# Kernel optimization log

Measured on AMD Instinct MI355X. Metric: run time of the kernel, lower is better.

Reference implementation:

```python
import jax, jax.numpy as jnp
import numpy as np

B, N, C, H = 2, 2048, 256, 8
HD = C // H
EPS = 1e-5


def _cdist(a, b):
    # a: (B,N,D), b: (B,M,D) -> (B,N,M) euclidean distance (torch.cdist p=2)
    d2 = (jnp.sum(a * a, -1)[:, :, None] + jnp.sum(b * b, -1)[:, None, :]
          - 2.0 * jnp.einsum('bnd,bmd->bnm', a, b))
    return jnp.sqrt(jnp.maximum(d2, 0.0))


def _ln(x, g, b):
    # LayerNorm over last axis
    m = jnp.mean(x, -1, keepdims=True)
    v = jnp.var(x, -1, keepdims=True)
    return (x - m) / jnp.sqrt(v + EPS) * g + b


def _conv1d(x, w, b=None):
    # 1x1 Conv1d: x (B,Cin,N), w (Cout,Cin)
    y = jnp.einsum('oc,bcn->bon', w, x)
    return y if b is None else y + b[:, None]


def setup_inputs() -> dict:
    key = jax.random.key(0)
    ks = jax.random.split(key, 32)
    s = 0.05
    inp = {
        'xyz_A': jax.random.normal(ks[0], (B, N, 3), jnp.float32),
        'featA': jax.random.normal(ks[1], (B, C, N), jnp.float32),
        'xyz_B': jax.random.normal(ks[2], (B, N, 3), jnp.float32),
        'featB': jax.random.normal(ks[3], (B, C, N), jnp.float32),
        # q/k/v projections (Conv1d 1x1)
        'qw': jax.random.normal(ks[4], (C, C), jnp.float32) * s,
        'qb': jnp.zeros((C,), jnp.float32),
        'kw': jax.random.normal(ks[5], (C, C), jnp.float32) * s,
        'kb': jnp.zeros((C,), jnp.float32),
        'vw': jax.random.normal(ks[6], (C, C), jnp.float32) * s,
        'vb': jnp.zeros((C,), jnp.float32),
        # spatial_bias_mlp: Conv2d(1,H/2,1,bias=False) -> BN2d(eval) -> ReLU -> Conv2d(H/2,H,1)
        'sbw1': jax.random.normal(ks[7], (H // 2,), jnp.float32) * s,
        'sbg': jnp.ones((H // 2,), jnp.float32),
        'sbb': jnp.zeros((H // 2,), jnp.float32),
        'sbm': jax.random.normal(ks[8], (H // 2,), jnp.float32) * 0.1,
        'sbv': jax.random.uniform(ks[9], (H // 2,), jnp.float32, 0.5, 1.5),
        'sbw2': jax.random.normal(ks[10], (H, H // 2), jnp.float32) * s,
        'sbb2': jnp.zeros((H,), jnp.float32),
        # dissimilarity projections
        'qdw': jax.random.normal(ks[11], (C, C), jnp.float32) * s,
        'qdb': jnp.zeros((C,), jnp.float32),
        'kdw': jax.random.normal(ks[12], (C, C), jnp.float32) * s,
        'kdb': jnp.zeros((C,), jnp.float32),
        # LayerNorms
        'lin_g': jnp.ones((C,), jnp.float32), 'lin_b': jnp.zeros((C,), jnp.float32),
        'lsim_g': jnp.ones((C,), jnp.float32), 'lsim_b': jnp.zeros((C,), jnp.float32),
        'ldis_g': jnp.ones((C,), jnp.float32), 'ldis_b': jnp.zeros((C,), jnp.float32),
        # fusion MLP: Conv1d(3C,2C,bias=False) -> BN1d(eval) -> ReLU -> Dropout(eval) -> Conv1d(2C,C)
        'fw1': jax.random.normal(ks[13], (2 * C, 3 * C), jnp.float32) * s,
        'fbg': jnp.ones((2 * C,), jnp.float32),
        'fbb': jnp.zeros((2 * C,), jnp.float32),
        'fbm': jax.random.normal(ks[14], (2 * C,), jnp.float32) * 0.1,
        'fbv': jax.random.uniform(ks[15], (2 * C,), jnp.float32, 0.5, 1.5),
        'fw2': jax.random.normal(ks[16], (C, 2 * C), jnp.float32) * s,
        'fb2': jnp.zeros((C,), jnp.float32),
    }
    return inp


def _forward(xyz_A, featA, xyz_B, featB, qw, qb, kw, kb, vw, vb,
             sbw1, sbg, sbb, sbm, sbv, sbw2, sbb2,
             qdw, qdb, kdw, kdb,
             lin_g, lin_b, lsim_g, lsim_b, ldis_g, ldis_b,
             fw1, fbg, fbb, fbm, fbv, fw2, fb2):
    # Pre-norm of featA over channels
    featA_norm = _ln(featA.transpose(0, 2, 1), lin_g, lin_b).transpose(0, 2, 1)  # (B,C,N)

    # Spatial bias: -cdist -> 1x1 conv (in_ch=1) -> BN(eval) -> ReLU -> 1x1 conv
    dist = _cdist(xyz_A, xyz_B)                                # (B,N,N)
    t = jnp.einsum('o,bnm->bonm', sbw1, -dist)                 # (B,H/2,N,N)
    t = (t - sbm[:, None, None]) / jnp.sqrt(sbv + EPS)[:, None, None]
    t = t * sbg[:, None, None] + sbb[:, None, None]
    t = jax.nn.relu(t)
    spatial_bias = jnp.einsum('oh,bhnm->bonm', sbw2, t) + sbb2[:, None, None]  # (B,H,N,N)

    # Similarity path
    q = _conv1d(featA_norm, qw, qb).reshape(B, H, HD, N).transpose(0, 1, 3, 2)  # (B,H,N,hd)
    k = _conv1d(featB, kw, kb).reshape(B, H, HD, N).transpose(0, 1, 3, 2)
    sim_scores = jnp.einsum('bhnd,bhmd->bhnm', q, k) / (HD ** 0.5) + spatial_bias

    # Dissimilarity path: feature cdist + spatial bias
    qd = _conv1d(featA_norm, qdw, qdb).transpose(0, 2, 1)      # (B,N,C)
    kd = _conv1d(featB, kdw, kdb).transpose(0, 2, 1)
    dissim_scores = _cdist(qd, kd)[:, None] + spatial_bias     # (B,H,N,N)

    sim_w = jax.nn.softmax(sim_scores, -1)
    dis_w = jax.nn.softmax(dissim_scores, -1)

    v = _conv1d(featB, vw, vb).reshape(B, H, HD, N).transpose(0, 1, 3, 2)       # (B,H,N,hd)
    ctx_sim = jnp.einsum('bhnm,bhmd->bhnd', sim_w, v).transpose(0, 1, 3, 2).reshape(B, C, N)
    ctx_sim = _ln(ctx_sim.transpose(0, 2, 1), lsim_g, lsim_b).transpose(0, 2, 1)
    ctx_dis = jnp.einsum('bhnm,bhmd->bhnd', dis_w, v).transpose(0, 1, 3, 2).reshape(B, C, N)
    ctx_dis = _ln(ctx_dis.transpose(0, 2, 1), ldis_g, ldis_b).transpose(0, 2, 1)

    fused = jnp.concatenate([featA_norm, ctx_sim, ctx_dis], axis=1)            # (B,3C,N)
    x = jnp.einsum('oc,bcn->bon', fw1, fused)
    x = (x - fbm[:, None]) / jnp.sqrt(fbv + EPS)[:, None] * fbg[:, None] + fbb[:, None]
    x = jax.nn.relu(x)  # Dropout is identity in eval mode
    out = _conv1d(x, fw2, fb2) + featA  # residual_proj is Identity (in==out)
    return out


def reference(xyz_A, featA, xyz_B, featB, qw, qb, kw, kb, vw, vb,
              sbw1, sbg, sbb, sbm, sbv, sbw2, sbb2,
              qdw, qdb, kdw, kdb,
              lin_g, lin_b, lsim_g, lsim_b, ldis_g, ldis_b,
              fw1, fbg, fbb, fbm, fbv, fw2, fb2):
    return _forward(xyz_A, featA, xyz_B, featB, qw, qb, kw, kb, vw, vb,
                    sbw1, sbg, sbb, sbm, sbv, sbw2, sbb2,
                    qdw, qdb, kdw, kdb,
                    lin_g, lin_b, lsim_g, lsim_b, ldis_g, ldis_b,
                    fw1, fbg, fbb, fbm, fbv, fw2, fb2)
```

## Files before the change

kernel.cpp:

```cpp
#include <hip/hip_runtime.h>

#define B_ 2
#define N_ 2048
#define C_ 256
#define H_ 8
#define HD_ 32
#define EPSf 1e-5f

typedef __bf16   bf16x8 __attribute__((ext_vector_type(8)));
typedef float    f32x4  __attribute__((ext_vector_type(4)));
typedef _Float16 f16x8  __attribute__((ext_vector_type(8)));
typedef _Float16 f16x4  __attribute__((ext_vector_type(4)));
typedef _Float16 f16x2  __attribute__((ext_vector_type(2)));

static constexpr size_t MB_ = 1024 * 1024;
static constexpr size_t OFF_FANT = 0;
static constexpr size_t OFF_FBT  = 2 * MB_;
static constexpr size_t OFF_QPK  = 4 * MB_;
static constexpr size_t OFF_KPK  = 6 * MB_;
static constexpr size_t OFF_VPK  = 8 * MB_;
static constexpr size_t OFF_QDT  = 10 * MB_;
static constexpr size_t OFF_KDT  = 12 * MB_;
static constexpr size_t OFF_QQ   = 14 * MB_;
static constexpr size_t OFF_KK   = 14 * MB_ + 16 * 1024;
static constexpr size_t OFF_FDH  = 14 * MB_ + 64 * 1024;
static constexpr size_t OFF_FSD  = 14 * MB_ + 64 * 1024;
static constexpr size_t OFF_CTXS = 31 * MB_;
static constexpr size_t OFF_CTXD = 35 * MB_;
static constexpr size_t OFF_CSLN = 39 * MB_;
static constexpr size_t OFF_CDLN = 41 * MB_;
static constexpr size_t OFF_X1T  = 43 * MB_;
static constexpr size_t WS_NEED  = 47 * MB_;
static constexpr size_t OFF2_CTXS = 47 * MB_;
static constexpr size_t OFF2_CTXD = 51 * MB_;
static constexpr size_t OFF2_CSLN = 55 * MB_;
static constexpr size_t OFF2_CDLN = 57 * MB_;
static constexpr size_t OFF2_X1T  = 59 * MB_;
static constexpr size_t WS_NEED2  = 63 * MB_;

__device__ __forceinline__ float rfl(float x){
  return __uint_as_float(__builtin_amdgcn_readfirstlane(__float_as_uint(x)));
}
__device__ __forceinline__ bf16x8 cvt8(const float* p){
  float4 a = *reinterpret_cast<const float4*>(p);
  float4 c = *reinterpret_cast<const float4*>(p + 4);
  bf16x8 r;
  r[0]=(__bf16)a.x; r[1]=(__bf16)a.y; r[2]=(__bf16)a.z; r[3]=(__bf16)a.w;
  r[4]=(__bf16)c.x; r[5]=(__bf16)c.y; r[6]=(__bf16)c.z; r[7]=(__bf16)c.w;
  return r;
}
__device__ __forceinline__ unsigned int packh2(float lo, float hi){
  f16x2 h; h[0] = (_Float16)lo; h[1] = (_Float16)hi;
  return __builtin_bit_cast(unsigned int, h);
}
__device__ __forceinline__ void unpackh2(unsigned int u, float& lo, float& hi){
  f16x2 h = __builtin_bit_cast(f16x2, u);
  lo = (float)h[0]; hi = (float)h[1];
}

__global__ __launch_bounds__(256) void lnA_pack(const float* __restrict__ featA,
    __bf16* __restrict__ fanT, const float* __restrict__ gam, const float* __restrict__ bet){
  int b = blockIdx.y, n0 = blockIdx.x * 32;
  int t = threadIdx.x, nl = t & 31, cg = t >> 5;
  __shared__ float tile[256][33];
  __shared__ float red1[8][32], red2[8][32], mus[32], rss[32];
  __shared__ float gsh[256], bsh[256];
  gsh[t] = gam[t]; bsh[t] = bet[t];
  #pragma unroll
  for (int i = 0; i < 32; i++){
    int c = cg * 32 + i;
    tile[c][nl] = featA[((size_t)(b * C_ + c)) * N_ + n0 + nl];
  }
  __syncthreads();
  float s1 = 0.f, s2 = 0.f;
  #pragma unroll
  for (int i = 0; i < 32; i++){
    float v = tile[cg * 32 + i][nl];
    s1 += v; s2 += v * v;
  }
  red1[cg][nl] = s1; red2[cg][nl] = s2;
  __syncthreads();
  if (t < 32){
    float a = 0.f, q = 0.f;
    #pragma unroll
    for (int i = 0; i < 8; i++){ a += red1[i][t]; q += red2[i][t]; }
    float m = a / (float)C_;
    mus[t] = m; rss[t] = rsqrtf(q / (float)C_ - m * m + EPSf);
  }
  __syncthreads();
  float mu = mus[nl], rs = rss[nl];
  size_t obase = ((size_t)(b * N_ + n0 + nl)) * C_;
  #pragma unroll
  for (int i = 0; i < 32; i++){
    int c = cg * 32 + i;
    fanT[obase + c] = (__bf16)((tile[c][nl] - mu) * rs * gsh[c] + bsh[c]);
  }
}

__global__ __launch_bounds__(256) void packT_kernel(const float* __restrict__ featB,
    __bf16* __restrict__ fbT){
  int b = blockIdx.z, c0 = blockIdx.y * 64, n0 = blockIdx.x * 64;
  int t = threadIdx.x;
  __shared__ float tile[64][65];
  int cl = t >> 6, nl = t & 63;
  #pragma unroll
  for (int i = 0; i < 16; i++)
    tile[i * 4 + cl][nl] = featB[((size_t)(b * C_ + c0 + i * 4 + cl)) * N_ + n0 + nl];
  __syncthreads();
  int nr = t >> 2, cc = (t & 3) * 16;
  alignas(16) __bf16 tmp[16];
  #pragma unroll
  for (int j = 0; j < 16; j++) tmp[j] = (__bf16)tile[cc + j][nr];
  size_t d = ((size_t)(b * N_ + n0 + nr)) * C_ + c0 + cc;
  *reinterpret_cast<uint4*>(&fbT[d])     = *reinterpret_cast<uint4*>(&tmp[0]);
  *reinterpret_cast<uint4*>(&fbT[d + 8]) = *reinterpret_cast<uint4*>(&tmp[8]);
}

__global__ __launch_bounds__(256) void proj_mfma(const __bf16* __restrict__ fanT,
    const __bf16* __restrict__ fbT, __bf16* __restrict__ wsh, int vfp16,
    const float* __restrict__ qw, const float* __restrict__ qb,
    const float* __restrict__ kw, const float* __restrict__ kb,
    const float* __restrict__ vw, const float* __restrict__ vb,
    const float* __restrict__ qdw, const float* __restrict__ qdb,
    const float* __restrict__ kdw, const float* __restrict__ kdb){
  const int p = blockIdx.z % 5, b = blockIdx.z / 5;
  const int t = threadIdx.x, w = t >> 6, lane = t & 63, ln = lane & 15, g = lane >> 4;
  const float *W, *bias;
  const __bf16* X;
  __bf16* Y;
  if (p == 0)      { W = qw;  bias = qb;  X = fanT; Y = wsh + (OFF_QPK - OFF_FANT) / 2; }
  else if (p == 1) { W = kw;  bias = kb;  X = fbT;  Y = wsh + (OFF_KPK - OFF_FANT) / 2; }
  else if (p == 2) { W = vw;  bias = vb;  X = fbT;  Y = wsh + (OFF_VPK - OFF_FANT) / 2; }
  else if (p == 3) { W = qdw; bias = qdb; X = fanT; Y = wsh + (OFF_QDT - OFF_FANT) / 2; }
  else             { W = kdw; bias = kdb; X = fbT;  Y = wsh + (OFF_KDT - OFF_FANT) / 2; }

  f32x4 acc[4];
  #pragma unroll
  for (int i = 0; i < 4; i++) acc[i] = (f32x4){0.f, 0.f, 0.f, 0.f};

  if (p != 2){
    const int n0w = blockIdx.x * 64 + w * 16, o0 = blockIdx.y * 64;
    #pragma unroll
    for (int ks = 0; ks < 8; ks++){
      bf16x8 af = *reinterpret_cast<const bf16x8*>(
          &X[((size_t)(b * N_ + n0w + ln)) * C_ + ks * 32 + g * 8]);
      #pragma unroll
      for (int ot = 0; ot < 4; ot++){
        bf16x8 bf = cvt8(&W[(size_t)(o0 + ot * 16 + ln) * C_ + ks * 32 + g * 8]);
        acc[ot] = __builtin_amdgcn_mfma_f32_16x16x32_bf16(af, bf, acc[ot], 0, 0, 0);
      }
    }
    const float inv = 0.17677669529663687f;
    #pragma unroll
    for (int ot = 0; ot < 4; ot++){
      int o = o0 + ot * 16 + ln;
      float bz = bias[o];
      #pragma unroll
      for (int r = 0; r < 4; r++){
        int n = n0w + g * 4 + r;
        float val = acc[ot][r] + bz;
        if (p == 0){
          val *= inv;
          Y[(((size_t)(b * H_ + (o >> 5))) * N_ + n) * HD_ + (o & 31)] = (__bf16)val;
        } else if (p == 1){
          Y[(((size_t)(b * H_ + (o >> 5))) * N_ + n) * HD_ + (o & 31)] = (__bf16)val;
        } else {
          Y[((size_t)(b * N_ + n)) * C_ + o] = (__bf16)val;
        }
      }
    }
  } else {
    const int o0w = blockIdx.y * 64 + w * 16, n0 = blockIdx.x * 64;
    #pragma unroll
    for (int ks = 0; ks < 8; ks++){
      bf16x8 af = cvt8(&W[(size_t)(o0w + ln) * C_ + ks * 32 + g * 8]);
      #pragma unroll
      for (int nt = 0; nt < 4; nt++){
        bf16x8 bf = *reinterpret_cast<const bf16x8*>(
            &X[((size_t)(b * N_ + n0 + nt * 16 + ln)) * C_ + ks * 32 + g * 8]);
        acc[nt] = __builtin_amdgcn_mfma_f32_16x16x32_bf16(af, bf, acc[nt], 0, 0, 0);
      }
    }
    float bz[4];
    #pragma unroll
    for (int r = 0; r < 4; r++) bz[r] = vb[o0w + g * 4 + r];
    #pragma unroll
    for (int nt = 0; nt < 4; nt++)
      #pragma unroll
      for (int r = 0; r < 4; r++){
        int o = o0w + g * 4 + r, n = n0 + nt * 16 + ln;
        size_t idx = ((size_t)(b * C_ + o)) * N_ + n;
        float val = acc[nt][r] + bz[r];
        if (vfp16) ((_Float16*)Y)[idx] = (_Float16)val;
        else       Y[idx] = (__bf16)val;
      }
  }
}

__global__ __launch_bounds__(256) void norms_b(const __bf16* __restrict__ qdT,
    const __bf16* __restrict__ kdT, float* __restrict__ qq, float* __restrict__ kk){
  int b = blockIdx.y, n = blockIdx.x * 64 + (threadIdx.x >> 2), part = threadIdx.x & 3;
  size_t base = ((size_t)(b * N_ + n)) * C_ + part * 64;
  float s1 = 0.f, s2 = 0.f;
  #pragma unroll
  for (int i = 0; i < 8; i++){
    bf16x8 a = *reinterpret_cast<const bf16x8*>(&qdT[base + i * 8]);
    bf16x8 d = *reinterpret_cast<const bf16x8*>(&kdT[base + i * 8]);
    #pragma unroll
    for (int j = 0; j < 8; j++){
      float fa = (float)a[j]; s1 += fa * fa;
      float fd = (float)d[j]; s2 += fd * fd;
    }
  }
  s1 += __shfl_xor(s1, 1); s1 += __shfl_xor(s1, 2);
  s2 += __shfl_xor(s2, 1); s2 += __shfl_xor(s2, 2);
  if (part == 0){ qq[b * N_ + n] = s1; kk[b * N_ + n] = s2; }
}

__global__ __launch_bounds__(256) void pairdist_mfma(const __bf16* __restrict__ qdT,
    const __bf16* __restrict__ kdT, const float* __restrict__ qq,
    const float* __restrict__ kk, const float* __restrict__ xyzA,
    const float* __restrict__ xyzB, unsigned int* __restrict__ fsd){
  const int t = threadIdx.x, w = t >> 6, lane = t & 63, ln = lane & 15, g = lane >> 4;
  const int b = blockIdx.z, n0 = blockIdx.y * 64, n0w = n0 + w * 16, m0 = blockIdx.x * 64;
  __shared__ float4 xa[64], xb[64];
  __shared__ unsigned int sbl[4][16][68];

  if (t < 64){
    const float* p = &xyzA[((size_t)(b * N_ + n0 + t)) * 3];
    xa[t] = make_float4(p[0], p[1], p[2], 0.f);
  } else if (t < 128){
    const float* p = &xyzB[((size_t)(b * N_ + m0 + t - 64)) * 3];
    xb[t - 64] = make_float4(p[0], p[1], p[2], 0.f);
  }
  bf16x8 qfr[8];
  #pragma unroll
  for (int ks = 0; ks < 8; ks++)
    qfr[ks] = *reinterpret_cast<const bf16x8*>(
        &qdT[((size_t)(b * N_ + n0w + ln)) * C_ + ks * 32 + g * 8]);
  float qqv[4];
  #pragma unroll
  for (int r = 0; r < 4; r++) qqv[r] = qq[b * N_ + n0w + g * 4 + r];
  __syncthreads();
  float4 xav[4];
  #pragma unroll
  for (int r = 0; r < 4; r++) xav[r] = xa[w * 16 + g * 4 + r];

  #pragma unroll
  for (int mt = 0; mt < 4; mt++){
    f32x4 a = (f32x4){0.f, 0.f, 0.f, 0.f};
    #pragma unroll
    for (int ks = 0; ks < 8; ks++){
      bf16x8 kfr = *reinterpret_cast<const bf16x8*>(
          &kdT[((size_t)(b * N_ + m0 + mt * 16 + ln)) * C_ + ks * 32 + g * 8]);
      a = __builtin_amdgcn_mfma_f32_16x16x32_bf16(qfr[ks], kfr, a, 0, 0, 0);
    }
    float kkv = kk[b * N_ + m0 + mt * 16 + ln];
    float4 xbv = xb[mt * 16 + ln];
    #pragma unroll
    for (int r = 0; r < 4; r++){
      float d2 = qqv[r] + kkv - 2.f * a[r];
      float fd = sqrtf(fmaxf(d2, 0.f));
      float dx = xav[r].x - xbv.x, dy = xav[r].y - xbv.y, dz = xav[r].z - xbv.z;
      float sd = sqrtf(dx * dx + dy * dy + dz * dz);
      sbl[w][g * 4 + r][mt * 16 + ln] = packh2(fd, sd);
    }
  }
  #pragma unroll
  for (int it = 0; it < 4; it++){
    int row = it * 4 + (lane >> 4), cq = lane & 15;
    uint4 v = *reinterpret_cast<const uint4*>(&sbl[w][row][cq * 4]);
    *reinterpret_cast<uint4*>(&fsd[((size_t)(b * N_ + n0w + row)) * N_ + m0 + cq * 4]) = v;
  }
}

__global__ __launch_bounds__(256) void dual_attn2(
    const __bf16* __restrict__ qpk, const __bf16* __restrict__ kpk,
    const _Float16* __restrict__ vph, const unsigned int* __restrict__ fsd,
    const float* __restrict__ sbw1, const float* __restrict__ sbg, const float* __restrict__ sbb,
    const float* __restrict__ sbm, const float* __restrict__ sbv,
    const float* __restrict__ sbw2, const float* __restrict__ sbb2,
    float* __restrict__ ctxsT, float* __restrict__ ctxdT){
  const int t = threadIdx.x, w = t >> 6, lane = t & 63, ln = lane & 15, g = lane >> 4;
  const int h = blockIdx.y, b = blockIdx.z;
  const int nbase = blockIdx.x * 64 + w * 16;
  const int n = nbase + ln;

  float Ac[4], Bc[4], W2h[4];
  #pragma unroll
  for (int j = 0; j < 4; j++){
    float rs = rsqrtf(sbv[j] + EPSf);
    Ac[j]  = rfl(-sbw1[j] * rs * sbg[j]);
    Bc[j]  = rfl(-sbm[j] * rs * sbg[j] + sbb[j]);
    W2h[j] = rfl(sbw2[h * 4 + j]);
  }
  float C0 = rfl(sbb2[h]);

  bf16x8 qf = *reinterpret_cast<const bf16x8*>(
      &qpk[(((size_t)(b * H_ + h)) * N_ + n) * HD_ + g * 8]);
  const unsigned int* fsdrow = &fsd[((size_t)(b * N_ + n)) * N_];
  const _Float16* vbase = &vph[((size_t)(b * C_ + h * HD_)) * N_];

  f32x4 os[2], od[2];
  #pragma unroll
  for (int i = 0; i < 2; i++){ os[i] = (f32x4){0.f,0.f,0.f,0.f}; od[i] = (f32x4){0.f,0.f,0.f,0.f}; }
  float ms = -3e38f, ls = 0.f, md = -3e38f, ld = 0.f;

  for (int m0 = 0; m0 < N_; m0 += 64){
    f32x4 sa[4];
    #pragma unroll
    for (int mt = 0; mt < 4; mt++){
      bf16x8 kf = *reinterpret_cast<const bf16x8*>(
          &kpk[(((size_t)(b * H_ + h)) * N_ + m0 + mt * 16 + ln) * HD_ + g * 8]);
      f32x4 z = (f32x4){0.f, 0.f, 0.f, 0.f};
      sa[mt] = __builtin_amdgcn_mfma_f32_16x16x32_bf16(kf, qf, z, 0, 0, 0);
    }
    float sv[16], dv[16];
    float mxs = -3e38f, mxd = -3e38f;
    #pragma unroll
    for (int mt = 0; mt < 4; mt++){
      uint4 fu = *reinterpret_cast<const uint4*>(&fsdrow[m0 + mt * 16 + g * 4]);
      #pragma unroll
      for (int r = 0; r < 4; r++){
        unsigned int uu = (r == 0) ? fu.x : (r == 1) ? fu.y : (r == 2) ? fu.z : fu.w;
        float fd, sd;
        unpackh2(uu, fd, sd);
        float u0 = fmaxf(fmaf(Ac[0], sd, Bc[0]), 0.f);
        float u1 = fmaxf(fmaf(Ac[1], sd, Bc[1]), 0.f);
        float u2 = fmaxf(fmaf(Ac[2], sd, Bc[2]), 0.f);
        float u3 = fmaxf(fmaf(Ac[3], sd, Bc[3]), 0.f);
        float bias = C0 + W2h[0] * u0 + W2h[1] * u1 + W2h[2] * u2 + W2h[3] * u3;
        float s = sa[mt][r] + bias;
        float d = fd + bias;
        sv[mt * 4 + r] = s; dv[mt * 4 + r] = d;
        mxs = fmaxf(mxs, s); mxd = fmaxf(mxd, d);
      }
    }
    mxs = fmaxf(mxs, __shfl_xor(mxs, 16)); mxs = fmaxf(mxs, __shfl_xor(mxs, 32));
    mxd = fmaxf(mxd, __shfl_xor(mxd, 16)); mxd = fmaxf(mxd, __shfl_xor(mxd, 32));
    float nms = fmaxf(ms, mxs), als = __expf(ms - nms);
    float nmd = fmaxf(md, mxd), ald = __expf(md - nmd);
    f16x4 pAs[4], pAd[4];
    float pss = 0.f, psd = 0.f;
    #pragma unroll
    for (int mt = 0; mt < 4; mt++)
      #pragma unroll
      for (int r = 0; r < 4; r++){
        float pv = __expf(sv[mt * 4 + r] - nms); pss += pv; pAs[mt][r] = (_Float16)pv;
        float qv = __expf(dv[mt * 4 + r] - nmd); psd += qv; pAd[mt][r] = (_Float16)qv;
      }
    pss += __shfl_xor(pss, 16); pss += __shfl_xor(pss, 32);
    psd += __shfl_xor(psd, 16); psd += __shfl_xor(psd, 32);
    ls = ls * als + pss; ms = nms;
    ld = ld * ald + psd; md = nmd;
    float alsr[4], aldr[4];
    #pragma unroll
    for (int r = 0; r < 4; r++){
      alsr[r] = __shfl(als, g * 4 + r);
      aldr[r] = __shfl(ald, g * 4 + r);
    }
    #pragma unroll
    for (int dt = 0; dt < 2; dt++)
      #pragma unroll
      for (int r = 0; r < 4; r++){ os[dt][r] *= alsr[r]; od[dt][r] *= aldr[r]; }
    #pragma unroll
    for (int mt = 0; mt < 4; mt++){
      #pragma unroll
      for (int dt = 0; dt < 2; dt++){
        f16x4 vf = *reinterpret_cast<const f16x4*>(
            &vbase[(size_t)(dt * 16 + ln) * N_ + m0 + mt * 16 + g * 4]);
        os[dt] = __builtin_amdgcn_mfma_f32_16x16x16f16(pAs[mt], vf, os[dt], 0, 0, 0);
        od[dt] = __builtin_amdgcn_mfma_f32_16x16x16f16(pAd[mt], vf, od[dt], 0, 0, 0);
      }
    }
  }
  float is = 1.f / ls, idd = 1.f / ld;
  float isr[4], idr[4];
  #pragma unroll
  for (int r = 0; r < 4; r++){
    isr[r] = __shfl(is, g * 4 + r);
    idr[r] = __shfl(idd, g * 4 + r);
  }
  #pragma unroll
  for (int dt = 0; dt < 2; dt++)
    #pragma unroll
    for (int r = 0; r < 4; r++){
      int nn = nbase + g * 4 + r;
      int ch = h * HD_ + dt * 16 + ln;
      size_t base = ((size_t)(b * N_ + nn)) * C_ + ch;
      ctxsT[base] = os[dt][r] * isr[r];
      ctxdT[base] = od[dt][r] * idr[r];
    }
}

__global__ __launch_bounds__(256) void fdist_mfma(const __bf16* __restrict__ qdT,
    const __bf16* __restrict__ kdT, const float* __restrict__ qq,
    const float* __restrict__ kk, _Float16* __restrict__ fdh){
  const int t = threadIdx.x, w = t >> 6, lane = t & 63, ln = lane & 15, g = lane >> 4;
  const int b = blockIdx.z, n0 = blockIdx.y * 64 + w * 16, m0 = blockIdx.x * 64;
  __shared__ _Float16 sbl[4][16][68];

  bf16x8 qfr[8];
  #pragma unroll
  for (int ks = 0; ks < 8; ks++)
    qfr[ks] = *reinterpret_cast<const bf16x8*>(
        &qdT[((size_t)(b * N_ + n0 + ln)) * C_ + ks * 32 + g * 8]);
  float qqv[4];
  #pragma unroll
  for (int r = 0; r < 4; r++) qqv[r] = qq[b * N_ + n0 + g * 4 + r];

  #pragma unroll
  for (int mt = 0; mt < 4; mt++){
    f32x4 a = (f32x4){0.f, 0.f, 0.f, 0.f};
    #pragma unroll
    for (int ks = 0; ks < 8; ks++){
      bf16x8 kfr = *reinterpret_cast<const bf16x8*>(
          &kdT[((size_t)(b * N_ + m0 + mt * 16 + ln)) * C_ + ks * 32 + g * 8]);
      a = __builtin_amdgcn_mfma_f32_16x16x32_bf16(qfr[ks], kfr, a, 0, 0, 0);
    }
    float kkv = kk[b * N_ + m0 + mt * 16 + ln];
    #pragma unroll
    for (int r = 0; r < 4; r++){
      float d2 = qqv[r] + kkv - 2.f * a[r];
      sbl[w][g * 4 + r][mt * 16 + ln] = (_Float16)sqrtf(fmaxf(d2, 0.f));
    }
  }
  __syncthreads();
  #pragma unroll
  for (int it = 0; it < 8; it++){
    int row = (lane >> 5) + it * 2, colu = lane & 31;
    unsigned int u = *reinterpret_cast<const unsigned int*>(&sbl[w][row][colu * 2]);
    *reinterpret_cast<unsigned int*>(&fdh[((size_t)(b * N_ + n0 + row)) * N_ + m0 + colu * 2]) = u;
  }
}

__global__ __launch_bounds__(256) void dual_attn(
    const __bf16* __restrict__ qpk, const __bf16* __restrict__ kpk, const __bf16* __restrict__ vpk,
    const _Float16* __restrict__ fdh,
    const float* __restrict__ xyzA, const float* __restrict__ xyzB,
    const float* __restrict__ sbw1, const float* __restrict__ sbg, const float* __restrict__ sbb,
    const float* __restrict__ sbm, const float* __restrict__ sbv,
    const float* __restrict__ sbw2, const float* __restrict__ sbb2,
    float* __restrict__ ctxsT, float* __restrict__ ctxdT){
  const int t = threadIdx.x, w = t >> 6, lane = t & 63, ln = lane & 15, g = lane >> 4;
  const int h = blockIdx.y, b = blockIdx.z;
  const int nbase = blockIdx.x * 64 + w * 16;
  const int n = nbase + ln;

  float Ac[4], Bc[4], W2h[4];
  #pragma unroll
  for (int j = 0; j < 4; j++){
    float rs = rsqrtf(sbv[j] + EPSf);
    Ac[j]  = rfl(-sbw1[j] * rs * sbg[j]);
    Bc[j]  = rfl(-sbm[j] * rs * sbg[j] + sbb[j]);
    W2h[j] = rfl(sbw2[h * 4 + j]);
  }
  float C0 = rfl(sbb2[h]);

  bf16x8 qf = *reinterpret_cast<const bf16x8*>(
      &qpk[(((size_t)(b * H_ + h)) * N_ + n) * HD_ + g * 8]);
  float ax = xyzA[((size_t)(b * N_ + n)) * 3 + 0];
  float ay = xyzA[((size_t)(b * N_ + n)) * 3 + 1];
  float az = xyzA[((size_t)(b * N_ + n)) * 3 + 2];
  const _Float16* fdrow = &fdh[((size_t)(b * N_ + n)) * N_];

  f32x4 os[2], od[2];
  #pragma unroll
  for (int i = 0; i < 2; i++){ os[i] = (f32x4){0.f,0.f,0.f,0.f}; od[i] = (f32x4){0.f,0.f,0.f,0.f}; }
  float ms = -3e38f, ls = 0.f, md = -3e38f, ld = 0.f;

  __shared__ __align__(16) float ss[4][16][68];
  __shared__ float4 xbb[4][64];

  for (int m0 = 0; m0 < N_; m0 += 64){
    __syncthreads();
    {
      const float* xp = &xyzB[((size_t)(b * N_ + m0 + lane)) * 3];
      xbb[w][lane] = make_float4(xp[0], xp[1], xp[2], 0.f);
    }
    f32x4 sa[4];
    #pragma unroll
    for (int i = 0; i < 4; i++) sa[i] = (f32x4){0.f, 0.f, 0.f, 0.f};
    #pragma unroll
    for (int mt = 0; mt < 4; mt++){
      bf16x8 kf = *reinterpret_cast<const bf16x8*>(
          &kpk[(((size_t)(b * H_ + h)) * N_ + m0 + mt * 16 + ln) * HD_ + g * 8]);
      sa[mt] = __builtin_amdgcn_mfma_f32_16x16x32_bf16(qf, kf, sa[mt], 0, 0, 0);
    }
    #pragma unroll
    for (int mt = 0; mt < 4; mt++)
      #pragma unroll
      for (int r = 0; r < 4; r++)
        ss[w][g * 4 + r][mt * 16 + ln] = sa[mt][r];
    __syncthreads();

    #pragma unroll
    for (int kh = 0; kh < 2; kh++){
      float s8[8], d8[8];
      {
        float4 A4 = *reinterpret_cast<const float4*>(&ss[w][ln][kh * 32 + g * 8]);
        float4 B4 = *reinterpret_cast<const float4*>(&ss[w][ln][kh * 32 + g * 8 + 4]);
        s8[0]=A4.x; s8[1]=A4.y; s8[2]=A4.z; s8[3]=A4.w;
        s8[4]=B4.x; s8[5]=B4.y; s8[6]=B4.z; s8[7]=B4.w;
      }
      f16x8 fv = *reinterpret_cast<const f16x8*>(&fdrow[m0 + kh * 32 + g * 8]);
      float mxs = -3e38f, mxd = -3e38f;
      #pragma unroll
      for (int j = 0; j < 8; j++){
        float4 xk = xbb[w][kh * 32 + g * 8 + j];
        float dx = ax - xk.x, dy = ay - xk.y, dz = az - xk.z;
        float sd = sqrtf(dx * dx + dy * dy + dz * dz);
        float bias = C0;
        #pragma unroll
        for (int u = 0; u < 4; u++)
          bias += W2h[u] * fmaxf(fmaf(Ac[u], sd, Bc[u]), 0.f);
        s8[j] += bias;
        d8[j] = (float)fv[j] + bias;
        mxs = fmaxf(mxs, s8[j]);
        mxd = fmaxf(mxd, d8[j]);
      }
      mxs = fmaxf(mxs, __shfl_xor(mxs, 16)); mxs = fmaxf(mxs, __shfl_xor(mxs, 32));
      mxd = fmaxf(mxd, __shfl_xor(mxd, 16)); mxd = fmaxf(mxd, __shfl_xor(mxd, 32));
      float nms = fmaxf(ms, mxs), als = __expf(ms - nms);
      float nmd = fmaxf(md, mxd), ald = __expf(md - nmd);
      float pss = 0.f, psd = 0.f;
      bf16x8 pfs, pfd;
      #pragma unroll
      for (int j = 0; j < 8; j++){
        float pv = __expf(s8[j] - nms); pss += pv; pfs[j] = (__bf16)pv;
        float qv = __expf(d8[j] - nmd); psd += qv; pfd[j] = (__bf16)qv;
      }
      pss += __shfl_xor(pss, 16); pss += __shfl_xor(pss, 32);
      psd += __shfl_xor(psd, 16); psd += __shfl_xor(psd, 32);
      ls = ls * als + pss; ms = nms;
      ld = ld * ald + psd; md = nmd;
      os[0] *= als; os[1] *= als; od[0] *= ald; od[1] *= ald;
      #pragma unroll
      for (int dt = 0; dt < 2; dt++){
        bf16x8 vf = *reinterpret_cast<const bf16x8*>(
            &vpk[((size_t)(b * C_ + h * HD_ + dt * 16 + ln)) * N_ + m0 + kh * 32 + g * 8]);
        os[dt] = __builtin_amdgcn_mfma_f32_16x16x32_bf16(vf, pfs, os[dt], 0, 0, 0);
        od[dt] = __builtin_amdgcn_mfma_f32_16x16x32_bf16(vf, pfd, od[dt], 0, 0, 0);
      }
    }
  }
  float is = 1.f / ls, idv = 1.f / ld;
  #pragma unroll
  for (int dt = 0; dt < 2; dt++)
    #pragma unroll
    for (int r = 0; r < 4; r++){
      int ch = h * HD_ + dt * 16 + g * 4 + r;
      size_t base = ((size_t)(b * N_ + n)) * C_ + ch;
      ctxsT[base] = os[dt][r] * is;
      ctxdT[base] = od[dt][r] * idv;
    }
}

__global__ __launch_bounds__(256) void ln_ctx(const float* __restrict__ ctxsT,
    const float* __restrict__ ctxdT, __bf16* __restrict__ csLN, __bf16* __restrict__ cdLN,
    const float* __restrict__ lsg, const float* __restrict__ lsb,
    const float* __restrict__ ldg, const float* __restrict__ ldb){
  const float* src = blockIdx.y ? ctxdT : ctxsT;
  __bf16* dst = blockIdx.y ? cdLN : csLN;
  const float* gg = blockIdx.y ? ldg : lsg;
  const float* bb = blockIdx.y ? ldb : lsb;
  int w = threadIdx.x >> 6, lane = threadIdx.x & 63;
  size_t row = (size_t)blockIdx.x * 4 + w;
  float4 v = *reinterpret_cast<const float4*>(&src[row * C_ + lane * 4]);
  float s1 = v.x + v.y + v.z + v.w;
  float s2 = v.x * v.x + v.y * v.y + v.z * v.z + v.w * v.w;
  #pragma unroll
  for (int off = 1; off < 64; off <<= 1){
    s1 += __shfl_xor(s1, off);
    s2 += __shfl_xor(s2, off);
  }
  float m = s1 / (float)C_;
  float rs = rsqrtf(s2 / (float)C_ - m * m + EPSf);
  float4 g4 = *reinterpret_cast<const float4*>(&gg[lane * 4]);
  float4 b4 = *reinterpret_cast<const float4*>(&bb[lane * 4]);
  alignas(8) __bf16 o4[4];
  o4[0] = (__bf16)((v.x - m) * rs * g4.x + b4.x);
  o4[1] = (__bf16)((v.y - m) * rs * g4.y + b4.y);
  o4[2] = (__bf16)((v.z - m) * rs * g4.z + b4.z);
  o4[3] = (__bf16)((v.w - m) * rs * g4.w + b4.w);
  *reinterpret_cast<uint2*>(&dst[row * C_ + lane * 4]) = *reinterpret_cast<uint2*>(o4);
}

__global__ __launch_bounds__(256) void fusion1_mfma(const __bf16* __restrict__ fanT,
    const __bf16* __restrict__ csLN, const __bf16* __restrict__ cdLN,
    __bf16* __restrict__ X1T, const float* __restrict__ fw1,
    const float* __restrict__ fbg, const float* __restrict__ fbb,
    const float* __restrict__ fbm, const float* __restrict__ fbv){
  const int t = threadIdx.x, w = t >> 6, lane = t & 63, ln = lane & 15, g = lane >> 4;
  const int b = blockIdx.z, o0 = blockIdx.y * 64, n0w = blockIdx.x * 64 + w * 16;
  f32x4 acc[4];
  #pragma unroll
  for (int i = 0; i < 4; i++) acc[i] = (f32x4){0.f, 0.f, 0.f, 0.f};
  const __bf16* segs[3] = {fanT, csLN, cdLN};
  #pragma unroll
  for (int ks = 0; ks < 24; ks++){
    const __bf16* base = segs[ks >> 3];
    int coff = (ks & 7) * 32 + g * 8;
    bf16x8 af = *reinterpret_cast<const bf16x8*>(
        &base[((size_t)(b * N_ + n0w + ln)) * C_ + coff]);
    #pragma unroll
    for (int ot = 0; ot < 4; ot++){
      bf16x8 bf = cvt8(&fw1[(size_t)(o0 + ot * 16 + ln) * (3 * C_) + ks * 32 + g * 8]);
      acc[ot] = __builtin_amdgcn_mfma_f32_16x16x32_bf16(af, bf, acc[ot], 0, 0, 0);
    }
  }
  #pragma unroll
  for (int ot = 0; ot < 4; ot++){
    int o = o0 + ot * 16 + ln;
    float mn = fbm[o], rs = rsqrtf(fbv[o] + EPSf), gg = fbg[o], be = fbb[o];
    #pragma unroll
    for (int r = 0; r < 4; r++){
      int n = n0w + g * 4 + r;
      float x = (acc[ot][r] - mn) * rs * gg + be;
      X1T[((size_t)(b * N_ + n)) * (2 * C_) + o] = (__bf16)fmaxf(x, 0.f);
    }
  }
}

__global__ __launch_bounds__(256) void fusion2_mfma(const __bf16* __restrict__ X1T,
    const float* __restrict__ fw2, const float* __restrict__ fb2,
    const float* __restrict__ featA, float* __restrict__ out){
  const int t = threadIdx.x, w = t >> 6, lane = t & 63, ln = lane & 15, g = lane >> 4;
  const int b = blockIdx.z, o0w = blockIdx.y * 64 + w * 16, n0 = blockIdx.x * 64;
  f32x4 acc[4];
  #pragma unroll
  for (int i = 0; i < 4; i++) acc[i] = (f32x4){0.f, 0.f, 0.f, 0.f};
  #pragma unroll
  for (int ks = 0; ks < 16; ks++){
    bf16x8 af = cvt8(&fw2[(size_t)(o0w + ln) * (2 * C_) + ks * 32 + g * 8]);
    #pragma unroll
    for (int nt = 0; nt < 4; nt++){
      bf16x8 bf = *reinterpret_cast<const bf16x8*>(
          &X1T[((size_t)(b * N_ + n0 + nt * 16 + ln)) * (2 * C_) + ks * 32 + g * 8]);
      acc[nt] = __builtin_amdgcn_mfma_f32_16x16x32_bf16(af, bf, acc[nt], 0, 0, 0);
    }
  }
  float bz[4];
  #pragma unroll
  for (int r = 0; r < 4; r++) bz[r] = fb2[o0w + g * 4 + r];
  #pragma unroll
  for (int nt = 0; nt < 4; nt++)
    #pragma unroll
    for (int r = 0; r < 4; r++){
      int o = o0w + g * 4 + r, n = n0 + nt * 16 + ln;
      size_t oi = ((size_t)(b * C_ + o)) * N_ + n;
      out[oi] = acc[nt][r] + bz[r] + featA[oi];
    }
}

extern "C" void kernel_launch(void* const* d_in, const int* in_sizes, int n_in,
                              void* d_out, int out_size, void* d_ws, size_t ws_size,
                              hipStream_t stream){
  (void)in_sizes; (void)n_in; (void)out_size;
  if (ws_size < WS_NEED) return;

  const float* xyzA  = (const float*)d_in[0];
  const float* featA = (const float*)d_in[1];
  const float* xyzB  = (const float*)d_in[2];
  const float* featB = (const float*)d_in[3];
  const float* qw  = (const float*)d_in[4];   const float* qb  = (const float*)d_in[5];
  const float* kw  = (const float*)d_in[6];   const float* kb  = (const float*)d_in[7];
  const float* vw  = (const float*)d_in[8];   const float* vb  = (const float*)d_in[9];
  const float* sbw1= (const float*)d_in[10];  const float* sbg = (const float*)d_in[11];
  const float* sbb = (const float*)d_in[12];  const float* sbm = (const float*)d_in[13];
  const float* sbv = (const float*)d_in[14];  const float* sbw2= (const float*)d_in[15];
  const float* sbb2= (const float*)d_in[16];
  const float* qdw = (const float*)d_in[17];  const float* qdb = (const float*)d_in[18];
  const float* kdw = (const float*)d_in[19];  const float* kdb = (const float*)d_in[20];
  const float* ling= (const float*)d_in[21];  const float* linb= (const float*)d_in[22];
  const float* lsg = (const float*)d_in[23];  const float* lsb = (const float*)d_in[24];
  const float* ldg = (const float*)d_in[25];  const float* ldb = (const float*)d_in[26];
  const float* fw1 = (const float*)d_in[27];  const float* fbg = (const float*)d_in[28];
  const float* fbb = (const float*)d_in[29];  const float* fbm = (const float*)d_in[30];
  const float* fbv = (const float*)d_in[31];  const float* fw2 = (const float*)d_in[32];
  const float* fb2 = (const float*)d_in[33];

  char* ws = (char*)d_ws;
  __bf16*   fanT = (__bf16*)(ws + OFF_FANT);
  __bf16*   fbT  = (__bf16*)(ws + OFF_FBT);
  __bf16*   qpk  = (__bf16*)(ws + OFF_QPK);
  __bf16*   kpk  = (__bf16*)(ws + OFF_KPK);
  __bf16*   qdT  = (__bf16*)(ws + OFF_QDT);
  __bf16*   kdT  = (__bf16*)(ws + OFF_KDT);
  float*    qq   = (float*)(ws + OFF_QQ);
  float*    kk   = (float*)(ws + OFF_KK);
  float*    out  = (float*)d_out;

  bool big = (ws_size >= WS_NEED2);

  lnA_pack<<<dim3(N_ / 32, B_), 256, 0, stream>>>(featA, fanT, ling, linb);
  packT_kernel<<<dim3(N_ / 64, C_ / 64, B_), 256, 0, stream>>>(featB, fbT);
  proj_mfma<<<dim3(N_ / 64, C_ / 64, 5 * B_), 256, 0, stream>>>(
      fanT, fbT, fanT, big ? 1 : 0, qw, qb, kw, kb, vw, vb, qdw, qdb, kdw, kdb);
  norms_b<<<dim3(N_ / 64, B_), 256, 0, stream>>>(qdT, kdT, qq, kk);

  if (big){
    _Float16*     vph  = (_Float16*)(ws + OFF_VPK);
    unsigned int* fsd  = (unsigned int*)(ws + OFF_FSD);
    float*  ctxsT = (float*)(ws + OFF2_CTXS);
    float*  ctxdT = (float*)(ws + OFF2_CTXD);
    __bf16* csLN  = (__bf16*)(ws + OFF2_CSLN);
    __bf16* cdLN  = (__bf16*)(ws + OFF2_CDLN);
    __bf16* X1T   = (__bf16*)(ws + OFF2_X1T);
    pairdist_mfma<<<dim3(N_ / 64, N_ / 64, B_), 256, 0, stream>>>(
        qdT, kdT, qq, kk, xyzA, xyzB, fsd);
    dual_attn2<<<dim3(N_ / 64, H_, B_), 256, 0, stream>>>(
        qpk, kpk, vph, fsd, sbw1, sbg, sbb, sbm, sbv, sbw2, sbb2, ctxsT, ctxdT);
    ln_ctx<<<dim3(B_ * N_ / 4, 2), 256, 0, stream>>>(
        ctxsT, ctxdT, csLN, cdLN, lsg, lsb, ldg, ldb);
    fusion1_mfma<<<dim3(N_ / 64, (2 * C_) / 64, B_), 256, 0, stream>>>(
        fanT, csLN, cdLN, X1T, fw1, fbg, fbb, fbm, fbv);
    fusion2_mfma<<<dim3(N_ / 64, C_ / 64, B_), 256, 0, stream>>>(
        X1T, fw2, fb2, featA, out);
  } else {
    __bf16*   vpk  = (__bf16*)(ws + OFF_VPK);
    _Float16* fdh  = (_Float16*)(ws + OFF_FDH);
    float*  ctxsT = (float*)(ws + OFF_CTXS);
    float*  ctxdT = (float*)(ws + OFF_CTXD);
    __bf16* csLN  = (__bf16*)(ws + OFF_CSLN);
    __bf16* cdLN  = (__bf16*)(ws + OFF_CDLN);
    __bf16* X1T   = (__bf16*)(ws + OFF_X1T);
    fdist_mfma<<<dim3(N_ / 64, N_ / 64, B_), 256, 0, stream>>>(qdT, kdT, qq, kk, fdh);
    dual_attn<<<dim3(N_ / 64, H_, B_), 256, 0, stream>>>(
        qpk, kpk, vpk, fdh, xyzA, xyzB,
        sbw1, sbg, sbb, sbm, sbv, sbw2, sbb2, ctxsT, ctxdT);
    ln_ctx<<<dim3(B_ * N_ / 4, 2), 256, 0, stream>>>(
        ctxsT, ctxdT, csLN, cdLN, lsg, lsb, ldg, ldb);
    fusion1_mfma<<<dim3(N_ / 64, (2 * C_) / 64, B_), 256, 0, stream>>>(
        fanT, csLN, cdLN, X1T, fw1, fbg, fbb, fbm, fbv);
    fusion2_mfma<<<dim3(N_ / 64, C_ / 64, B_), 256, 0, stream>>>(
        X1T, fw2, fb2, featA, out);
  }
}
```

Measured before the change: 291.1 us.

## Split attention key range in two with register double-buffering and merged combine+LayerNorm

```diff
diff --git a/kernel.cpp b/kernel.cpp
--- a/kernel.cpp
+++ b/kernel.cpp
@@ -31,12 +31,13 @@
 static constexpr size_t OFF_CDLN = 41 * MB_;
 static constexpr size_t OFF_X1T  = 43 * MB_;
 static constexpr size_t WS_NEED  = 47 * MB_;
-static constexpr size_t OFF2_CTXS = 47 * MB_;
-static constexpr size_t OFF2_CTXD = 51 * MB_;
-static constexpr size_t OFF2_CSLN = 55 * MB_;
-static constexpr size_t OFF2_CDLN = 57 * MB_;
-static constexpr size_t OFF2_X1T  = 59 * MB_;
-static constexpr size_t WS_NEED2  = 63 * MB_;
+static constexpr size_t OFF2_PART  = 47 * MB_;
+static constexpr size_t OFF2_STATM = 55 * MB_;
+static constexpr size_t OFF2_STATL = 56 * MB_;
+static constexpr size_t OFF2_CSLN  = 15 * MB_;
+static constexpr size_t OFF2_CDLN  = 17 * MB_;
+static constexpr size_t OFF2_X1T   = 19 * MB_;
+static constexpr size_t WS_NEED2   = 63 * MB_;
 
 __device__ __forceinline__ float rfl(float x){
   return __uint_as_float(__builtin_amdgcn_readfirstlane(__float_as_uint(x)));
@@ -274,17 +275,104 @@
   }
 }
 
-__global__ __launch_bounds__(256) void dual_attn2(
+struct TileRegs { uint4 fu[4]; bf16x8 kf[4]; };
+
+__device__ __forceinline__ void load_tile(TileRegs& T, const __bf16* kbase,
+    const unsigned int* fsdrow, int m0, int ln, int g){
+  #pragma unroll
+  for (int mt = 0; mt < 4; mt++){
+    T.fu[mt] = *reinterpret_cast<const uint4*>(&fsdrow[m0 + mt * 16 + g * 4]);
+    T.kf[mt] = *reinterpret_cast<const bf16x8*>(&kbase[(size_t)(m0 + mt * 16 + ln) * HD_ + g * 8]);
+  }
+}
+
+__device__ __forceinline__ void compute_tile(const TileRegs& T,
+    const _Float16* vbase, int m0, int ln, int g, bf16x8 qf,
+    const float* Ac, const float* Bc, const float* W2h, float C0,
+    f32x4* os, f32x4* od, float& ms, float& ls, float& md, float& ld){
+  f32x4 sa[4];
+  #pragma unroll
+  for (int mt = 0; mt < 4; mt++){
+    f32x4 z = (f32x4){0.f, 0.f, 0.f, 0.f};
+    sa[mt] = __builtin_amdgcn_mfma_f32_16x16x32_bf16(T.kf[mt], qf, z, 0, 0, 0);
+  }
+  f16x4 vf[2][4];
+  #pragma unroll
+  for (int mt = 0; mt < 4; mt++)
+    #pragma unroll
+    for (int dt = 0; dt < 2; dt++)
+      vf[dt][mt] = *reinterpret_cast<const f16x4*>(
+          &vbase[(size_t)(dt * 16 + ln) * N_ + m0 + mt * 16 + g * 4]);
+  f32x4 dvv[4];
+  float mxs = -3e38f, mxd = -3e38f;
+  #pragma unroll
+  for (int mt = 0; mt < 4; mt++){
+    #pragma unroll
+    for (int r = 0; r < 4; r++){
+      unsigned int uu = (r == 0) ? T.fu[mt].x : (r == 1) ? T.fu[mt].y
+                      : (r == 2) ? T.fu[mt].z : T.fu[mt].w;
+      float fd, sd;
+      unpackh2(uu, fd, sd);
+      float u0 = fmaxf(fmaf(Ac[0], sd, Bc[0]), 0.f);
+      float u1 = fmaxf(fmaf(Ac[1], sd, Bc[1]), 0.f);
+      float u2 = fmaxf(fmaf(Ac[2], sd, Bc[2]), 0.f);
+      float u3 = fmaxf(fmaf(Ac[3], sd, Bc[3]), 0.f);
+      float bias = C0 + W2h[0] * u0 + W2h[1] * u1 + W2h[2] * u2 + W2h[3] * u3;
+      float s = sa[mt][r] + bias;
+      float d = fd + bias;
+      sa[mt][r] = s; dvv[mt][r] = d;
+      mxs = fmaxf(mxs, s); mxd = fmaxf(mxd, d);
+    }
+  }
+  mxs = fmaxf(mxs, __shfl_xor(mxs, 16)); mxs = fmaxf(mxs, __shfl_xor(mxs, 32));
+  mxd = fmaxf(mxd, __shfl_xor(mxd, 16)); mxd = fmaxf(mxd, __shfl_xor(mxd, 32));
+  float nms = fmaxf(ms, mxs), als = __expf(ms - nms);
+  float nmd = fmaxf(md, mxd), ald = __expf(md - nmd);
+  f16x4 pAs[4], pAd[4];
+  float pss = 0.f, psd = 0.f;
+  #pragma unroll
+  for (int mt = 0; mt < 4; mt++)
+    #pragma unroll
+    for (int r = 0; r < 4; r++){
+      float pv = __expf(sa[mt][r] - nms); pss += pv; pAs[mt][r] = (_Float16)pv;
+      float qv = __expf(dvv[mt][r] - nmd); psd += qv; pAd[mt][r] = (_Float16)qv;
+    }
+  pss += __shfl_xor(pss, 16); pss += __shfl_xor(pss, 32);
+  psd += __shfl_xor(psd, 16); psd += __shfl_xor(psd, 32);
+  ls = ls * als + pss; ms = nms;
+  ld = ld * ald + psd; md = nmd;
+  float alsr[4], aldr[4];
+  #pragma unroll
+  for (int r = 0; r < 4; r++){
+    alsr[r] = __shfl(als, g * 4 + r);
+    aldr[r] = __shfl(ald, g * 4 + r);
+  }
+  #pragma unroll
+  for (int dt = 0; dt < 2; dt++)
+    #pragma unroll
+    for (int r = 0; r < 4; r++){ os[dt][r] *= alsr[r]; od[dt][r] *= aldr[r]; }
+  #pragma unroll
+  for (int mt = 0; mt < 4; mt++)
+    #pragma unroll
+    for (int dt = 0; dt < 2; dt++){
+      os[dt] = __builtin_amdgcn_mfma_f32_16x16x16f16(pAs[mt], vf[dt][mt], os[dt], 0, 0, 0);
+      od[dt] = __builtin_amdgcn_mfma_f32_16x16x16f16(pAd[mt], vf[dt][mt], od[dt], 0, 0, 0);
+    }
+}
+
+__global__ __launch_bounds__(256) void dual_attn3(
     const __bf16* __restrict__ qpk, const __bf16* __restrict__ kpk,
     const _Float16* __restrict__ vph, const unsigned int* __restrict__ fsd,
     const float* __restrict__ sbw1, const float* __restrict__ sbg, const float* __restrict__ sbb,
     const float* __restrict__ sbm, const float* __restrict__ sbv,
     const float* __restrict__ sbw2, const float* __restrict__ sbb2,
-    float* __restrict__ ctxsT, float* __restrict__ ctxdT){
+    _Float16* __restrict__ partO, float* __restrict__ statM, float* __restrict__ statL){
   const int t = threadIdx.x, w = t >> 6, lane = t & 63, ln = lane & 15, g = lane >> 4;
-  const int h = blockIdx.y, b = blockIdx.z;
+  const int h = blockIdx.y;
+  const int b = blockIdx.z >> 1, split = blockIdx.z & 1;
   const int nbase = blockIdx.x * 64 + w * 16;
   const int n = nbase + ln;
+  const int mstart = split * (N_ / 2);
 
   float Ac[4], Bc[4], W2h[4];
   #pragma unroll
@@ -299,6 +387,7 @@
   bf16x8 qf = *reinterpret_cast<const bf16x8*>(
       &qpk[(((size_t)(b * H_ + h)) * N_ + n) * HD_ + g * 8]);
   const unsigned int* fsdrow = &fsd[((size_t)(b * N_ + n)) * N_];
+  const __bf16* kbase = &kpk[(((size_t)(b * H_ + h)) * N_) * HD_];
   const _Float16* vbase = &vph[((size_t)(b * C_ + h * HD_)) * N_];
 
   f32x4 os[2], od[2];
@@ -306,74 +395,16 @@
   for (int i = 0; i < 2; i++){ os[i] = (f32x4){0.f,0.f,0.f,0.f}; od[i] = (f32x4){0.f,0.f,0.f,0.f}; }
   float ms = -3e38f, ls = 0.f, md = -3e38f, ld = 0.f;
 
-  for (int m0 = 0; m0 < N_; m0 += 64){
-    f32x4 sa[4];
-    #pragma unroll
-    for (int mt = 0; mt < 4; mt++){
-      bf16x8 kf = *reinterpret_cast<const bf16x8*>(
-          &kpk[(((size_t)(b * H_ + h)) * N_ + m0 + mt * 16 + ln) * HD_ + g * 8]);
-      f32x4 z = (f32x4){0.f, 0.f, 0.f, 0.f};
-      sa[mt] = __builtin_amdgcn_mfma_f32_16x16x32_bf16(kf, qf, z, 0, 0, 0);
-    }
-    float sv[16], dv[16];
-    float mxs = -3e38f, mxd = -3e38f;
-    #pragma unroll
-    for (int mt = 0; mt < 4; mt++){
-      uint4 fu = *reinterpret_cast<const uint4*>(&fsdrow[m0 + mt * 16 + g * 4]);
-      #pragma unroll
-      for (int r = 0; r < 4; r++){
-        unsigned int uu = (r == 0) ? fu.x : (r == 1) ? fu.y : (r == 2) ? fu.z : fu.w;
-        float fd, sd;
-        unpackh2(uu, fd, sd);
-        float u0 = fmaxf(fmaf(Ac[0], sd, Bc[0]), 0.f);
-        float u1 = fmaxf(fmaf(Ac[1], sd, Bc[1]), 0.f);
-        float u2 = fmaxf(fmaf(Ac[2], sd, Bc[2]), 0.f);
-        float u3 = fmaxf(fmaf(Ac[3], sd, Bc[3]), 0.f);
-        float bias = C0 + W2h[0] * u0 + W2h[1] * u1 + W2h[2] * u2 + W2h[3] * u3;
-        float s = sa[mt][r] + bias;
-        float d = fd + bias;
-        sv[mt * 4 + r] = s; dv[mt * 4 + r] = d;
-        mxs = fmaxf(mxs, s); mxd = fmaxf(mxd, d);
-      }
-    }
-    mxs = fmaxf(mxs, __shfl_xor(mxs, 16)); mxs = fmaxf(mxs, __shfl_xor(mxs, 32));
-    mxd = fmaxf(mxd, __shfl_xor(mxd, 16)); mxd = fmaxf(mxd, __shfl_xor(mxd, 32));
-    float nms = fmaxf(ms, mxs), als = __expf(ms - nms);
-    float nmd = fmaxf(md, mxd), ald = __expf(md - nmd);
-    f16x4 pAs[4], pAd[4];
-    float pss = 0.f, psd = 0.f;
-    #pragma unroll
-    for (int mt = 0; mt < 4; mt++)
-      #pragma unroll
-      for (int r = 0; r < 4; r++){
-        float pv = __expf(sv[mt * 4 + r] - nms); pss += pv; pAs[mt][r] = (_Float16)pv;
-        float qv = __expf(dv[mt * 4 + r] - nmd); psd += qv; pAd[mt][r] = (_Float16)qv;
-      }
-    pss += __shfl_xor(pss, 16); pss += __shfl_xor(pss, 32);
-    psd += __shfl_xor(psd, 16); psd += __shfl_xor(psd, 32);
-    ls = ls * als + pss; ms = nms;
-    ld = ld * ald + psd; md = nmd;
-    float alsr[4], aldr[4];
-    #pragma unroll
-    for (int r = 0; r < 4; r++){
-      alsr[r] = __shfl(als, g * 4 + r);
-      aldr[r] = __shfl(ald, g * 4 + r);
-    }
-    #pragma unroll
-    for (int dt = 0; dt < 2; dt++)
-      #pragma unroll
-      for (int r = 0; r < 4; r++){ os[dt][r] *= alsr[r]; od[dt][r] *= aldr[r]; }
-    #pragma unroll
-    for (int mt = 0; mt < 4; mt++){
-      #pragma unroll
-      for (int dt = 0; dt < 2; dt++){
-        f16x4 vf = *reinterpret_cast<const f16x4*>(
-            &vbase[(size_t)(dt * 16 + ln) * N_ + m0 + mt * 16 + g * 4]);
-        os[dt] = __builtin_amdgcn_mfma_f32_16x16x16f16(pAs[mt], vf, os[dt], 0, 0, 0);
-        od[dt] = __builtin_amdgcn_mfma_f32_16x16x16f16(pAd[mt], vf, od[dt], 0, 0, 0);
-      }
-    }
-  }
+  TileRegs TA, TB;
+  load_tile(TA, kbase, fsdrow, mstart, ln, g);
+  for (int i = 0; i < 16; i += 2){
+    int m0 = mstart + i * 64;
+    load_tile(TB, kbase, fsdrow, m0 + 64, ln, g);
+    compute_tile(TA, vbase, m0, ln, g, qf, Ac, Bc, W2h, C0, os, od, ms, ls, md, ld);
+    if (i + 2 < 16) load_tile(TA, kbase, fsdrow, m0 + 128, ln, g);
+    compute_tile(TB, vbase, m0 + 64, ln, g, qf, Ac, Bc, W2h, C0, os, od, ms, ls, md, ld);
+  }
+
   float is = 1.f / ls, idd = 1.f / ld;
   float isr[4], idr[4];
   #pragma unroll
@@ -387,10 +418,67 @@
     for (int r = 0; r < 4; r++){
       int nn = nbase + g * 4 + r;
       int ch = h * HD_ + dt * 16 + ln;
-      size_t base = ((size_t)(b * N_ + nn)) * C_ + ch;
-      ctxsT[base] = os[dt][r] * isr[r];
-      ctxdT[base] = od[dt][r] * idr[r];
-    }
+      size_t p0 = (((size_t)(0 * 2 + split) * B_ + b) * N_ + nn) * C_ + ch;
+      size_t p1 = (((size_t)(2 + split) * B_ + b) * N_ + nn) * C_ + ch;
+      partO[p0] = (_Float16)(os[dt][r] * isr[r]);
+      partO[p1] = (_Float16)(od[dt][r] * idr[r]);
+    }
+  if (lane < 16){
+    int nn = nbase + lane;
+    size_t s0 = (((size_t)(0 * 2 + split) * B_ + b) * H_ + h) * N_ + nn;
+    size_t s1 = (((size_t)(2 + split) * B_ + b) * H_ + h) * N_ + nn;
+    statM[s0] = ms; statL[s0] = ls;
+    statM[s1] = md; statL[s1] = ld;
+  }
+}
+
+__global__ __launch_bounds__(256) void combine_ln(
+    const _Float16* __restrict__ partO, const float* __restrict__ statM,
+    const float* __restrict__ statL, __bf16* __restrict__ csLN, __bf16* __restrict__ cdLN,
+    const float* __restrict__ lsg, const float* __restrict__ lsb,
+    const float* __restrict__ ldg, const float* __restrict__ ldb){
+  const int path = blockIdx.y;
+  const int w = threadIdx.x >> 6, lane = threadIdx.x & 63;
+  const size_t row = (size_t)blockIdx.x * 4 + w;
+  const int b = (int)(row >> 11), n = (int)(row & (N_ - 1));
+  const int h = lane >> 3;
+  const float* gg = path ? ldg : lsg;
+  const float* bb = path ? ldb : lsb;
+  __bf16* dst = path ? cdLN : csLN;
+
+  size_t pb0 = (((size_t)(path * 2 + 0) * B_ + b) * N_ + n) * C_ + lane * 4;
+  size_t pb1 = (((size_t)(path * 2 + 1) * B_ + b) * N_ + n) * C_ + lane * 4;
+  f16x4 p0 = *reinterpret_cast<const f16x4*>(&partO[pb0]);
+  f16x4 p1 = *reinterpret_cast<const f16x4*>(&partO[pb1]);
+  size_t sb0 = (((size_t)(path * 2 + 0) * B_ + b) * H_ + h) * N_ + n;
+  size_t sb1 = (((size_t)(path * 2 + 1) * B_ + b) * H_ + h) * N_ + n;
+  float m0 = statM[sb0], l0 = statL[sb0];
+  float m1 = statM[sb1], l1 = statL[sb1];
+  float M = fmaxf(m0, m1);
+  float w0 = l0 * __expf(m0 - M), w1 = l1 * __expf(m1 - M);
+  float inv = 1.f / (w0 + w1);
+  float o[4];
+  #pragma unroll
+  for (int j = 0; j < 4; j++)
+    o[j] = (w0 * (float)p0[j] + w1 * (float)p1[j]) * inv;
+
+  float s1 = o[0] + o[1] + o[2] + o[3];
+  float s2 = o[0]*o[0] + o[1]*o[1] + o[2]*o[2] + o[3]*o[3];
+  #pragma unroll
+  for (int off = 1; off < 64; off <<= 1){
+    s1 += __shfl_xor(s1, off);
+    s2 += __shfl_xor(s2, off);
+  }
+  float mu = s1 / (float)C_;
+  float rs = rsqrtf(s2 / (float)C_ - mu * mu + EPSf);
+  float4 g4 = *reinterpret_cast<const float4*>(&gg[lane * 4]);
+  float4 b4 = *reinterpret_cast<const float4*>(&bb[lane * 4]);
+  alignas(8) __bf16 o4[4];
+  o4[0] = (__bf16)((o[0] - mu) * rs * g4.x + b4.x);
+  o4[1] = (__bf16)((o[1] - mu) * rs * g4.y + b4.y);
+  o4[2] = (__bf16)((o[2] - mu) * rs * g4.z + b4.z);
+  o4[3] = (__bf16)((o[3] - mu) * rs * g4.w + b4.w);
+  *reinterpret_cast<uint2*>(&dst[row * C_ + lane * 4]) = *reinterpret_cast<uint2*>(o4);
 }
 
 __global__ __launch_bounds__(256) void fdist_mfma(const __bf16* __restrict__ qdT,
@@ -702,17 +790,19 @@
   if (big){
     _Float16*     vph  = (_Float16*)(ws + OFF_VPK);
     unsigned int* fsd  = (unsigned int*)(ws + OFF_FSD);
-    float*  ctxsT = (float*)(ws + OFF2_CTXS);
-    float*  ctxdT = (float*)(ws + OFF2_CTXD);
-    __bf16* csLN  = (__bf16*)(ws + OFF2_CSLN);
-    __bf16* cdLN  = (__bf16*)(ws + OFF2_CDLN);
-    __bf16* X1T   = (__bf16*)(ws + OFF2_X1T);
+    _Float16* partO = (_Float16*)(ws + OFF2_PART);
+    float*    statM = (float*)(ws + OFF2_STATM);
+    float*    statL = (float*)(ws + OFF2_STATL);
+    __bf16*   csLN  = (__bf16*)(ws + OFF2_CSLN);
+    __bf16*   cdLN  = (__bf16*)(ws + OFF2_CDLN);
+    __bf16*   X1T   = (__bf16*)(ws + OFF2_X1T);
     pairdist_mfma<<<dim3(N_ / 64, N_ / 64, B_), 256, 0, stream>>>(
         qdT, kdT, qq, kk, xyzA, xyzB, fsd);
-    dual_attn2<<<dim3(N_ / 64, H_, B_), 256, 0, stream>>>(
-        qpk, kpk, vph, fsd, sbw1, sbg, sbb, sbm, sbv, sbw2, sbb2, ctxsT, ctxdT);
-    ln_ctx<<<dim3(B_ * N_ / 4, 2), 256, 0, stream>>>(
-        ctxsT, ctxdT, csLN, cdLN, lsg, lsb, ldg, ldb);
+    dual_attn3<<<dim3(N_ / 64, H_, B_ * 2), 256, 0, stream>>>(
+        qpk, kpk, vph, fsd, sbw1, sbg, sbb, sbm, sbv, sbw2, sbb2,
+        partO, statM, statL);
+    combine_ln<<<dim3(B_ * N_ / 4, 2), 256, 0, stream>>>(
+        partO, statM, statL, csLN, cdLN, lsg, lsb, ldg, ldb);
     fusion1_mfma<<<dim3(N_ / 64, (2 * C_) / 64, B_), 256, 0, stream>>>(
         fanT, csLN, cdLN, X1T, fw1, fbg, fbb, fbm, fbv);
     fusion2_mfma<<<dim3(N_ / 64, C_ / 64, B_), 256, 0, stream>>>(
```

Measured after the change: 270.9 us. 6.9% less time.
